# Kernel optimization log

Measured on AMD Instinct MI355X. Metric: run time of the kernel, lower is better.

The kernel has to match this reference:

```python
import jax, jax.numpy as jnp
import numpy as np

H = 32  # hidden_size
I = 1   # input_size
O = 12  # fc output

def setup_inputs() -> dict:
    key = jax.random.key(0)
    ks = jax.random.split(key, 8)
    B, T = 4096, 512
    s_ih = 1.0 / np.sqrt(H)
    x = jax.random.normal(ks[0], (B, T, I), dtype=jnp.float32)
    w_ih = jax.random.uniform(ks[1], (3 * H, I), minval=-s_ih, maxval=s_ih, dtype=jnp.float32)
    w_hh = jax.random.uniform(ks[2], (3 * H, H), minval=-s_ih, maxval=s_ih, dtype=jnp.float32)
    b_ih = jax.random.uniform(ks[3], (3 * H,), minval=-s_ih, maxval=s_ih, dtype=jnp.float32)
    b_hh = jax.random.uniform(ks[4], (3 * H,), minval=-s_ih, maxval=s_ih, dtype=jnp.float32)
    s_fc = 1.0 / np.sqrt(H)
    fc_w = jax.random.uniform(ks[5], (O, H), minval=-s_fc, maxval=s_fc, dtype=jnp.float32)
    fc_b = jax.random.uniform(ks[6], (O,), minval=-s_fc, maxval=s_fc, dtype=jnp.float32)
    return {"x": x, "w_ih": w_ih, "w_hh": w_hh, "b_ih": b_ih, "b_hh": b_hh, "fc_w": fc_w, "fc_b": fc_b}

def _gru_last_hidden(x, w_ih, w_hh, b_ih, b_hh):
    # x: [B, T, I]. Precompute input projections for all timesteps: [B, T, 3H]
    gi = jnp.einsum('bti,gi->btg', x, w_ih) + b_ih
    gi = jnp.swapaxes(gi, 0, 1)  # [T, B, 3H] for scan over time
    B = x.shape[0]
    h0 = jnp.zeros((B, H), dtype=x.dtype)

    def step(h, gi_t):
        gh = h @ w_hh.T + b_hh  # [B, 3H]
        i_r, i_z, i_n = jnp.split(gi_t, 3, axis=-1)
        h_r, h_z, h_n = jnp.split(gh, 3, axis=-1)
        r = jax.nn.sigmoid(i_r + h_r)
        z = jax.nn.sigmoid(i_z + h_z)
        n = jnp.tanh(i_n + r * h_n)
        h_new = (1.0 - z) * n + z * h
        return h_new, None

    h_last, _ = jax.lax.scan(step, h0, gi)
    return h_last  # [B, H]

def reference(x, w_ih, w_hh, b_ih, b_hh, fc_w, fc_b):
    h_last = _gru_last_hidden(x, w_ih, w_hh, b_ih, b_hh)
    return h_last @ fc_w.T + fc_b  # [B, 12]
```

## Files before the change

### kernel.cpp

```cpp
#include <hip/hip_runtime.h>


namespace {

typedef _Float16 f16;
typedef _Float16 f16x8 __attribute__((ext_vector_type(8)));
typedef float    f32x4 __attribute__((ext_vector_type(4)));

constexpr int kT = 512;
constexpr float kL2E = 1.4426950408889634f;

__device__ __forceinline__ float fast_exp2(float a) {
#if __has_builtin(__builtin_amdgcn_exp2f)
    return __builtin_amdgcn_exp2f(a);
#else
    return exp2f(a);
#endif
}
__device__ __forceinline__ float fast_rcp(float a) {
#if __has_builtin(__builtin_amdgcn_rcpf)
    return __builtin_amdgcn_rcpf(a);
#else
    return 1.0f / a;
#endif
}

__device__ __forceinline__ float sel4(const f32x4& a, bool b0, bool b1) {
    const float x01 = b0 ? a[1] : a[0];
    const float x23 = b0 ? a[3] : a[2];
    return b1 ? x23 : x01;
}

__global__ __launch_bounds__(128)
__attribute__((amdgpu_waves_per_eu(2, 2)))
void gru_2wb(
    const float* __restrict__ x,
    const float* __restrict__ w_ih,
    const float* __restrict__ w_hh,
    const float* __restrict__ b_ih,
    const float* __restrict__ b_hh,
    const float* __restrict__ fc_w,
    const float* __restrict__ fc_b,
    float* __restrict__ out)
{
    __shared__ f16   hbuf[2][4][32];
    __shared__ float hf[4 * 33];

    const int tid  = threadIdx.x;
    const int w    = tid >> 6;
    const int lane = tid & 63;
    const int c    = lane & 15;
    const int lg   = lane >> 4;
    const int q    = c >> 2;
    const int j    = c & 3;
    const int blk  = blockIdx.x;

    f16x8 wA[3];
#pragma unroll
    for (int g = 0; g < 3; ++g) {
        const float s = (g < 2) ? -kL2E : 2.0f * kL2E;
        f16x8 f;
#pragma unroll
        for (int i = 0; i < 8; ++i)
            f[i] = (f16)(s * w_hh[(g * 32 + w * 16 + c) * 32 + 8 * lg + i]);
        wA[g] = f;
    }

    f32x4 biasC[3];
#pragma unroll
    for (int v = 0; v < 4; ++v) {
        const int u = w * 16 + 4 * lg + v;
        biasC[0][v] = -kL2E * (b_ih[u] + b_hh[u]);
        biasC[1][v] = -kL2E * (b_ih[u + 32] + b_hh[u + 32]);
        biasC[2][v] = 2.0f * kL2E * b_hh[u + 64];
    }

    const int u = w * 16 + 4 * lg + q;
    const float cwr = -kL2E * w_ih[u];
    const float cwz = -kL2E * w_ih[u + 32];
    const float cwn = 2.0f * kL2E * w_ih[u + 64];
    const float cbn = 2.0f * kL2E * b_ih[u + 64];
    const bool b0 = (q & 1) != 0;
    const bool b1 = (q & 2) != 0;

    float h = 0.0f;
    f16x8 B = {(f16)0, (f16)0, (f16)0, (f16)0,
               (f16)0, (f16)0, (f16)0, (f16)0};

    const float4* xrow = reinterpret_cast<const float4*>(
        x + ((size_t)blk * 4 + j) * kT);
    float4 xcur = xrow[0];

    for (int t0 = 0; t0 < kT; t0 += 4) {
        const int nq = (t0 + 4 < kT) ? (t0 >> 2) + 1 : (t0 >> 2);
        float4 xnext = xrow[nq];

#pragma unroll
        for (int tt = 0; tt < 4; ++tt) {
            const float xt = (tt == 0) ? xcur.x : (tt == 1) ? xcur.y
                           : (tt == 2) ? xcur.z : xcur.w;
            const int buf = tt & 1;

            const f32x4 aR = __builtin_amdgcn_mfma_f32_16x16x32_f16(wA[0], B, biasC[0], 0, 0, 0);
            const f32x4 aZ = __builtin_amdgcn_mfma_f32_16x16x32_f16(wA[1], B, biasC[1], 0, 0, 0);
            const f32x4 aN = __builtin_amdgcn_mfma_f32_16x16x32_f16(wA[2], B, biasC[2], 0, 0, 0);

            const float pr = sel4(aR, b0, b1);
            const float pz = sel4(aZ, b0, b1);
            const float pn = sel4(aN, b0, b1);
            const float ar  = fmaf(xt, cwr, pr);
            const float az  = fmaf(xt, cwz, pz);
            const float inn = fmaf(xt, cwn, cbn);
            const float sr = 1.0f + fast_exp2(ar);
            const float sz = 1.0f + fast_exp2(az);
            const float ip = fast_rcp(sr * sz);
            const float r  = ip * sz;
            const float z  = ip * sr;
            const float n = fmaf(-2.0f,
                fast_rcp(1.0f + fast_exp2(fmaf(r, pn, inn))), 1.0f);
            h = fmaf(z, h - n, n);

            hbuf[buf][j][u] = (f16)h;
            asm volatile("s_waitcnt lgkmcnt(0)" ::: "memory");
            __builtin_amdgcn_s_barrier();
            B = *reinterpret_cast<const f16x8*>(&hbuf[buf][j][8 * lg]);
        }
        xcur = xnext;
    }

    hf[j * 33 + u] = h;
    __syncthreads();
    if (tid < 48) {
        const int row = tid / 12, o = tid % 12;
        float acc = fc_b[o];
#pragma unroll
        for (int k = 0; k < 32; ++k)
            acc = fmaf(fc_w[o * 32 + k], hf[row * 33 + k], acc);
        out[((size_t)blk * 4 + row) * 12 + o] = acc;
    }
}

}

extern "C" void kernel_launch(void* const* d_in, const int* in_sizes, int n_in,
                              void* d_out, int out_size, void* d_ws, size_t ws_size,
                              hipStream_t stream) {
    const float* x    = (const float*)d_in[0];
    const float* w_ih = (const float*)d_in[1];
    const float* w_hh = (const float*)d_in[2];
    const float* b_ih = (const float*)d_in[3];
    const float* b_hh = (const float*)d_in[4];
    const float* fc_w = (const float*)d_in[5];
    const float* fc_b = (const float*)d_in[6];
    float* out = (float*)d_out;

    dim3 grid(1024);
    dim3 block(128);
    gru_2wb<<<grid, block, 0, stream>>>(x, w_ih, w_hh, b_ih, b_hh, fc_w, fc_b, out);
}
```

Baseline: 108.8 us.

## Process two independent batch chains per workgroup to interleave GRU recurrences

Each workgroup now advances two independent 4-sequence batches (A and B) through the recurrence together, issuing six MFMAs per step and sharing one barrier per timestep. The grid is halved to 512 blocks and waves_per_eu is set to 1. The aim is to hide MFMA and transcendental latency on the serial dependency chain through instruction-level parallelism, and to amortize barrier cost across two chains. In exchange, register pressure rises and occupancy and total wave-level parallelism drop, so fewer blocks share each CU.

```diff
diff --git a/kernel.cpp b/kernel.cpp
--- a/kernel.cpp
+++ b/kernel.cpp
@@ -32,8 +32,8 @@
 }
 
 __global__ __launch_bounds__(128)
-__attribute__((amdgpu_waves_per_eu(2, 2)))
-void gru_2wb(
+__attribute__((amdgpu_waves_per_eu(1, 1)))
+void gru_2w2c(
     const float* __restrict__ x,
     const float* __restrict__ w_ih,
     const float* __restrict__ w_hh,
@@ -43,8 +43,9 @@
     const float* __restrict__ fc_b,
     float* __restrict__ out)
 {
-    __shared__ f16   hbuf[2][4][32];
-    __shared__ float hf[4 * 33];
+    __shared__ f16   hbufA[2][4][32];
+    __shared__ f16   hbufB[2][4][32];
+    __shared__ float hf[8 * 33];
 
     const int tid  = threadIdx.x;
     const int w    = tid >> 6;
@@ -83,60 +84,92 @@
     const bool b0 = (q & 1) != 0;
     const bool b1 = (q & 2) != 0;
 
-    float h = 0.0f;
-    f16x8 B = {(f16)0, (f16)0, (f16)0, (f16)0,
-               (f16)0, (f16)0, (f16)0, (f16)0};
+    float hA = 0.0f, hB = 0.0f;
+    f16x8 BA = {(f16)0, (f16)0, (f16)0, (f16)0,
+                (f16)0, (f16)0, (f16)0, (f16)0};
+    f16x8 BB = BA;
 
-    const float4* xrow = reinterpret_cast<const float4*>(
-        x + ((size_t)blk * 4 + j) * kT);
-    float4 xcur = xrow[0];
+    const float4* xrowA = reinterpret_cast<const float4*>(
+        x + ((size_t)blk * 8 + j) * kT);
+    const float4* xrowB = reinterpret_cast<const float4*>(
+        x + ((size_t)blk * 8 + 4 + j) * kT);
+    float4 xcurA = xrowA[0];
+    float4 xcurB = xrowB[0];
 
     for (int t0 = 0; t0 < kT; t0 += 4) {
         const int nq = (t0 + 4 < kT) ? (t0 >> 2) + 1 : (t0 >> 2);
-        float4 xnext = xrow[nq];
+        float4 xnextA = xrowA[nq];
+        float4 xnextB = xrowB[nq];
 
 #pragma unroll
         for (int tt = 0; tt < 4; ++tt) {
-            const float xt = (tt == 0) ? xcur.x : (tt == 1) ? xcur.y
-                           : (tt == 2) ? xcur.z : xcur.w;
+            const float xtA = (tt == 0) ? xcurA.x : (tt == 1) ? xcurA.y
+                            : (tt == 2) ? xcurA.z : xcurA.w;
+            const float xtB = (tt == 0) ? xcurB.x : (tt == 1) ? xcurB.y
+                            : (tt == 2) ? xcurB.z : xcurB.w;
             const int buf = tt & 1;
 
-            const f32x4 aR = __builtin_amdgcn_mfma_f32_16x16x32_f16(wA[0], B, biasC[0], 0, 0, 0);
-            const f32x4 aZ = __builtin_amdgcn_mfma_f32_16x16x32_f16(wA[1], B, biasC[1], 0, 0, 0);
-            const f32x4 aN = __builtin_amdgcn_mfma_f32_16x16x32_f16(wA[2], B, biasC[2], 0, 0, 0);
+            const f32x4 aRA = __builtin_amdgcn_mfma_f32_16x16x32_f16(wA[0], BA, biasC[0], 0, 0, 0);
+            const f32x4 aRB = __builtin_amdgcn_mfma_f32_16x16x32_f16(wA[0], BB, biasC[0], 0, 0, 0);
+            const f32x4 aZA = __builtin_amdgcn_mfma_f32_16x16x32_f16(wA[1], BA, biasC[1], 0, 0, 0);
+            const f32x4 aZB = __builtin_amdgcn_mfma_f32_16x16x32_f16(wA[1], BB, biasC[1], 0, 0, 0);
+            const f32x4 aNA = __builtin_amdgcn_mfma_f32_16x16x32_f16(wA[2], BA, biasC[2], 0, 0, 0);
+            const f32x4 aNB = __builtin_amdgcn_mfma_f32_16x16x32_f16(wA[2], BB, biasC[2], 0, 0, 0);
 
-            const float pr = sel4(aR, b0, b1);
-            const float pz = sel4(aZ, b0, b1);
-            const float pn = sel4(aN, b0, b1);
-            const float ar  = fmaf(xt, cwr, pr);
-            const float az  = fmaf(xt, cwz, pz);
-            const float inn = fmaf(xt, cwn, cbn);
-            const float sr = 1.0f + fast_exp2(ar);
-            const float sz = 1.0f + fast_exp2(az);
-            const float ip = fast_rcp(sr * sz);
-            const float r  = ip * sz;
-            const float z  = ip * sr;
-            const float n = fmaf(-2.0f,
-                fast_rcp(1.0f + fast_exp2(fmaf(r, pn, inn))), 1.0f);
-            h = fmaf(z, h - n, n);
+            {
+                const float pr = sel4(aRA, b0, b1);
+                const float pz = sel4(aZA, b0, b1);
+                const float pn = sel4(aNA, b0, b1);
+                const float ar  = fmaf(xtA, cwr, pr);
+                const float az  = fmaf(xtA, cwz, pz);
+                const float inn = fmaf(xtA, cwn, cbn);
+                const float sr = 1.0f + fast_exp2(ar);
+                const float sz = 1.0f + fast_exp2(az);
+                const float ip = fast_rcp(sr * sz);
+                const float r  = ip * sz;
+                const float z  = ip * sr;
+                const float n = fmaf(-2.0f,
+                    fast_rcp(1.0f + fast_exp2(fmaf(r, pn, inn))), 1.0f);
+                hA = fmaf(z, hA - n, n);
+            }
+            {
+                const float pr = sel4(aRB, b0, b1);
+                const float pz = sel4(aZB, b0, b1);
+                const float pn = sel4(aNB, b0, b1);
+                const float ar  = fmaf(xtB, cwr, pr);
+                const float az  = fmaf(xtB, cwz, pz);
+                const float inn = fmaf(xtB, cwn, cbn);
+                const float sr = 1.0f + fast_exp2(ar);
+                const float sz = 1.0f + fast_exp2(az);
+                const float ip = fast_rcp(sr * sz);
+                const float r  = ip * sz;
+                const float z  = ip * sr;
+                const float n = fmaf(-2.0f,
+                    fast_rcp(1.0f + fast_exp2(fmaf(r, pn, inn))), 1.0f);
+                hB = fmaf(z, hB - n, n);
+            }
 
-            hbuf[buf][j][u] = (f16)h;
+            hbufA[buf][j][u] = (f16)hA;
+            hbufB[buf][j][u] = (f16)hB;
             asm volatile("s_waitcnt lgkmcnt(0)" ::: "memory");
             __builtin_amdgcn_s_barrier();
-            B = *reinterpret_cast<const f16x8*>(&hbuf[buf][j][8 * lg]);
+            BA = *reinterpret_cast<const f16x8*>(&hbufA[buf][j][8 * lg]);
+            BB = *reinterpret_cast<const f16x8*>(&hbufB[buf][j][8 * lg]);
         }
-        xcur = xnext;
+        xcurA = xnextA;
+        xcurB = xnextB;
     }
 
-    hf[j * 33 + u] = h;
+    hf[j * 33 + u]       = hA;
+    hf[(j + 4) * 33 + u] = hB;
     __syncthreads();
-    if (tid < 48) {
+    if (tid < 96) {
         const int row = tid / 12, o = tid % 12;
         float acc = fc_b[o];
 #pragma unroll
         for (int k = 0; k < 32; ++k)
             acc = fmaf(fc_w[o * 32 + k], hf[row * 33 + k], acc);
-        out[((size_t)blk * 4 + row) * 12 + o] = acc;
+        out[((size_t)blk * 8 + row) * 12 + o] = acc;
     }
 }
 
@@ -154,7 +187,7 @@
     const float* fc_b = (const float*)d_in[6];
     float* out = (float*)d_out;
 
-    dim3 grid(1024);
+    dim3 grid(512);
     dim3 block(128);
-    gru_2wb<<<grid, block, 0, stream>>>(x, w_ih, w_hh, b_ih, b_hh, fc_w, fc_b, out);
+    gru_2w2c<<<grid, block, 0, stream>>>(x, w_ih, w_hh, b_ih, b_hh, fc_w, fc_b, out);
 }
```

New measurement: 150.6 us. +38.4%, slower.
